# Kernel tuning notes

Measured on AMD Instinct MI355X. Metric: run time of the kernel, lower is better.

## Reference

```python
import jax, jax.numpy as jnp
import numpy as np

BATCH, SEQ, HIDDEN = 8, 2048, 2048
N_FREQS = SEQ // 2 + 1  # 1025


def setup_inputs() -> dict:
    key = jax.random.key(0)
    k_x, k_w, k_b = jax.random.split(key, 3)
    x = jax.random.normal(k_x, (BATCH, SEQ, HIDDEN), dtype=jnp.float32)
    # Params per __init__: gate init ones/zeros; Linear(hidden, hidden)
    gate_real = jnp.ones((N_FREQS, HIDDEN), dtype=jnp.float32)
    gate_imag = jnp.zeros((N_FREQS, HIDDEN), dtype=jnp.float32)
    bound = 1.0 / np.sqrt(HIDDEN)
    W = jax.random.uniform(k_w, (HIDDEN, HIDDEN), minval=-bound, maxval=bound, dtype=jnp.float32)
    b = jax.random.uniform(k_b, (HIDDEN,), minval=-bound, maxval=bound, dtype=jnp.float32)
    return {"x": x, "gate_real": gate_real, "gate_imag": gate_imag, "W": W, "b": b}


def reference(x, gate_real, gate_imag, W, b):
    # x: (batch, seq, hidden)
    seq_len = x.shape[1]
    x_fft = jnp.fft.rfft(x, axis=1)  # (batch, n_freqs, hidden) complex64
    n_freqs = x_fft.shape[1]
    gate = gate_real[:n_freqs] + 1j * gate_imag[:n_freqs]  # (n_freqs, hidden)
    x_fft = x_fft * gate
    y = jnp.fft.irfft(x_fft, n=seq_len, axis=1)  # (batch, seq, hidden) float32
    # out_proj: y @ W.T + b  (torch Linear convention, W: (out, in))
    out = jnp.einsum('bsh,oh->bso', y, W) + b
    return out
```

## Files before the change

kernel.cpp:

```cpp
#include <hip/hip_runtime.h>
#include <math.h>

typedef __attribute__((ext_vector_type(8))) short bf16x8;
typedef __attribute__((ext_vector_type(4))) float f32x4;

__device__ __forceinline__ unsigned short f2bf(float f) {
  unsigned int u = __float_as_uint(f);
  unsigned int r = (u + 0x7fffu + ((u >> 16) & 1u)) >> 16;
  return (unsigned short)r;
}
__device__ __forceinline__ unsigned int pack2bf(float a, float b) {
  return (unsigned int)f2bf(a) | ((unsigned int)f2bf(b) << 16);
}
__device__ __forceinline__ float bflo(unsigned int g) { return __uint_as_float(g << 16); }
__device__ __forceinline__ float bfhi(unsigned int g) { return __uint_as_float(g & 0xffff0000u); }

__device__ __forceinline__ void glds16(const void* gp, void* lp) {
  __builtin_amdgcn_global_load_lds(
      (const __attribute__((address_space(1))) void*)gp,
      (__attribute__((address_space(3))) void*)lp, 16, 0, 0);
}

__device__ __constant__ float CW16[16] = {
  1.0f, 0.9807852804032304f, 0.9238795325112867f, 0.8314696123025452f,
  0.7071067811865476f, 0.5555702330196022f, 0.3826834323650898f, 0.19509032201612828f,
  0.0f, -0.19509032201612828f, -0.3826834323650898f, -0.5555702330196022f,
  -0.7071067811865476f, -0.8314696123025452f, -0.9238795325112867f, -0.9807852804032304f};
__device__ __constant__ float SW16[16] = {
  0.0f, 0.19509032201612828f, 0.3826834323650898f, 0.5555702330196022f,
  0.7071067811865476f, 0.8314696123025452f, 0.9238795325112867f, 0.9807852804032304f,
  1.0f, 0.9807852804032304f, 0.9238795325112867f, 0.8314696123025452f,
  0.7071067811865476f, 0.5555702330196022f, 0.3826834323650898f, 0.19509032201612828f};
__device__ __constant__ int BR5[32] = {
  0,16,8,24,4,20,12,28,2,18,10,26,6,22,14,30,
  1,17,9,25,5,21,13,29,3,19,11,27,7,23,15,31};

__device__ __forceinline__ int bitrev6(int l) {
  return ((l&1)<<5)|((l&2)<<3)|((l&4)<<1)|((l&8)>>1)|((l&16)>>3)|((l&32)>>5);
}

__device__ __forceinline__ float hsin(float rev) { return __builtin_amdgcn_sinf(rev); }
__device__ __forceinline__ float hcos(float rev) { return __builtin_amdgcn_cosf(rev); }

__device__ __forceinline__ void fwd_core(float (&ur)[32], float (&ui)[32], const int lane) {
  #pragma unroll
  for (int s = 0; s < 6; ++s) {
    const int h = 32 >> s;
    const int j = lane & (h - 1);
    const float rev = (float)j * (0.5f / (float)h);
    const bool hi = (lane & h) != 0;
    const float c  = hi ? hcos(rev) : 1.0f;
    const float sv = hi ? hsin(rev) : 0.0f;
    const float sgn = hi ? -1.0f : 1.0f;
    #pragma unroll
    for (int r = 0; r < 32; ++r) {
      float pr = __shfl_xor(ur[r], h, 64);
      float pi = __shfl_xor(ui[r], h, 64);
      float tr = fmaf(sgn, ur[r], pr);
      float ti = fmaf(sgn, ui[r], pi);
      ur[r] = fmaf(ti, sv, tr * c);
      ui[r] = fmaf(-tr, sv, ti * c);
    }
  }
  const int kap = bitrev6(lane);
  #pragma unroll
  for (int j = 1; j < 32; ++j) {
    const float rev = (float)(j * kap) * (1.0f / 2048.0f);
    const float sn = hsin(rev), cs = hcos(rev);
    float t = ur[j] * cs + ui[j] * sn;
    ui[j] = ui[j] * cs - ur[j] * sn;
    ur[j] = t;
  }
  #pragma unroll
  for (int s = 0; s < 5; ++s) {
    const int h = 16 >> s;
    #pragma unroll
    for (int i = 0; i < 32; ++i) if (!(i & h)) {
      const int tw = (i & (h - 1)) * (16 / h);
      float dr = ur[i] - ur[i + h], di = ui[i] - ui[i + h];
      ur[i] += ur[i + h]; ui[i] += ui[i + h];
      ur[i + h] = dr * CW16[tw] + di * SW16[tw];
      ui[i + h] = di * CW16[tw] - dr * SW16[tw];
    }
  }
}

__device__ __forceinline__ void inv_core(float (&ur)[32], float (&ui)[32], const int lane) {
  const int kap = bitrev6(lane);
  #pragma unroll
  for (int s = 0; s < 5; ++s) {
    const int h = 1 << s;
    #pragma unroll
    for (int i = 0; i < 32; ++i) if (!(i & h)) {
      const int tw = (i & (h - 1)) * (16 / h);
      float tr2 = ur[i + h] * CW16[tw] - ui[i + h] * SW16[tw];
      float ti2 = ui[i + h] * CW16[tw] + ur[i + h] * SW16[tw];
      ur[i + h] = ur[i] - tr2; ui[i + h] = ui[i] - ti2;
      ur[i] += tr2; ui[i] += ti2;
    }
  }
  #pragma unroll
  for (int j = 1; j < 32; ++j) {
    const float rev = (float)(j * kap) * (1.0f / 2048.0f);
    const float sn = hsin(rev), cs = hcos(rev);
    float t = ur[j] * cs - ui[j] * sn;
    ui[j] = ui[j] * cs + ur[j] * sn;
    ur[j] = t;
  }
  #pragma unroll
  for (int s = 0; s < 6; ++s) {
    const int h = 1 << s;
    const int j = lane & (h - 1);
    const float rev = (float)j * (0.5f / (float)h);
    const bool hi = (lane & h) != 0;
    const float c  = hi ? hcos(rev) : 1.0f;
    const float sv = hi ? hsin(rev) : 0.0f;
    const float sgn = hi ? -1.0f : 1.0f;
    #pragma unroll
    for (int r = 0; r < 32; ++r) {
      float vr = fmaf(-ui[r], sv, ur[r] * c);
      float vi = fmaf(ur[r], sv, ui[r] * c);
      float pvr = __shfl_xor(vr, h, 64);
      float pvi = __shfl_xor(vi, h, 64);
      ur[r] = fmaf(sgn, vr, pvr);
      ui[r] = fmaf(sgn, vi, pvi);
    }
  }
}

__global__ __launch_bounds__(256) void gate_pack_k(const float* __restrict__ gr,
                                                   const float* __restrict__ gi,
                                                   unsigned int* __restrict__ gt) {
  __shared__ float tr[32][33];
  __shared__ float ti[32][33];
  const int t = threadIdx.x;
  const int k0 = blockIdx.x * 32, hb = blockIdx.y * 32;
  const int hx = t & 31, fr = t >> 5;
  #pragma unroll
  for (int p = 0; p < 4; ++p) {
    int ff = p * 8 + fr;
    int k = k0 + ff;
    int f = (k <= 1024) ? k : (2048 - k);
    float sg = (k <= 1024) ? 1.f : -1.f;
    tr[ff][hx] = gr[(size_t)f * 2048 + hb + hx] * (1.f / 2048.f);
    ti[ff][hx] = sg * gi[(size_t)f * 2048 + hb + hx] * (1.f / 2048.f);
  }
  __syncthreads();
  const int kk = t & 31, hr = t >> 5;
  #pragma unroll
  for (int p = 0; p < 4; ++p) {
    int hl = p * 8 + hr;
    float re = tr[kk][hl], im = ti[kk][hl];
    gt[(size_t)(hb + hl) * 2048 + k0 + kk] =
        (unsigned int)f2bf(re) | ((unsigned int)f2bf(im) << 16);
  }
}

__global__ __launch_bounds__(256) void gate_ab_k(const float* __restrict__ gr,
                                                 const float* __restrict__ gi,
                                                 uint2* __restrict__ ab) {
  __shared__ unsigned int uA[32][33];
  __shared__ unsigned int uB[32][33];
  const int t = threadIdx.x;
  const int k0 = blockIdx.x * 32, h0 = blockIdx.y * 32;
  const int c = t & 31, r = t >> 5;
  #pragma unroll
  for (int pp = 0; pp < 4; ++pp) {
    const int kk = pp * 8 + r;
    const int k = k0 + kk;
    const int h = h0 + c;
    const float gkr = gr[(size_t)k * 2048 + h];
    const float gki = gi[(size_t)k * 2048 + h];
    const float gcr = gr[(size_t)(1024 - k) * 2048 + h];
    const float gci = gi[(size_t)(1024 - k) * 2048 + h];
    const float inv = 1.0f / 1024.0f;
    float Ar, Ai, Br, Bi;
    if (k == 0) {
      Ar = (gkr + gcr) * 0.5f * inv; Ai = 0.f;
      Br = 0.f; Bi = (gkr - gcr) * 0.5f * inv;
    } else {
      const float rev = (float)k * (1.0f / 2048.0f);
      const float sn = hsin(rev), cs = hcos(rev);
      const float Sr = (gkr + gcr) * 0.5f, Si = (gki - gci) * 0.5f;
      const float Dr = (gkr - gcr) * 0.5f, Di = (gki + gci) * 0.5f;
      Ar = (Sr - sn * Dr) * inv; Ai = (Si - sn * Di) * inv;
      Br = (-cs * Di) * inv;     Bi = (cs * Dr) * inv;
    }
    uA[kk][c] = pack2bf(Ar, Ai);
    uB[kk][c] = pack2bf(Br, Bi);
  }
  __syncthreads();
  #pragma unroll
  for (int pp = 0; pp < 4; ++pp) {
    const int hh = pp * 8 + r;
    ab[(size_t)(h0 + hh) * 1024 + k0 + c] = make_uint2(uA[c][hh], uB[c][hh]);
  }
}

__global__ __launch_bounds__(256) void wconv_k(const float* __restrict__ W,
                                               unsigned short* __restrict__ Wb) {
  int i = blockIdx.x * 256 + threadIdx.x;
  float4 v = ((const float4*)W)[i];
  ushort4 o;
  o.x = f2bf(v.x); o.y = f2bf(v.y); o.z = f2bf(v.z); o.w = f2bf(v.w);
  ((ushort4*)Wb)[i] = o;
}

__global__ __launch_bounds__(256) void xtrans_k(const float* __restrict__ x,
                                                float* __restrict__ xT) {
  __shared__ float t[32][33];
  const int b = blockIdx.z;
  const int s0 = blockIdx.x * 32, h0 = blockIdx.y * 32;
  const float* xb = x + ((size_t)b * 2048) * 2048;
  float* xTb = xT + ((size_t)b * 2048) * 2048;
  const int c = threadIdx.x & 31, r = threadIdx.x >> 5;
  #pragma unroll
  for (int p = 0; p < 4; ++p) {
    int rr = p * 8 + r;
    t[rr][c] = xb[(size_t)(s0 + rr) * 2048 + h0 + c];
  }
  __syncthreads();
  #pragma unroll
  for (int p = 0; p < 4; ++p) {
    int rr = p * 8 + r;
    xTb[(size_t)(h0 + rr) * 2048 + s0 + c] = t[c][rr];
  }
}

__global__ __launch_bounds__(256) void ytrans_k(const unsigned short* __restrict__ yT,
                                                unsigned short* __restrict__ y) {
  __shared__ unsigned short t[64][66];
  const int b = blockIdx.z;
  const int h0 = blockIdx.x * 64, s0 = blockIdx.y * 64;
  const unsigned short* src = yT + ((size_t)b * 2048 + h0) * 2048 + s0;
  unsigned short* dst = y + ((size_t)b * 2048 + s0) * 2048 + h0;
  const int c = threadIdx.x & 15, r = threadIdx.x >> 4;
  #pragma unroll
  for (int p = 0; p < 4; ++p) {
    int rr = p * 16 + r;
    ushort4 v = *(const ushort4*)(src + (size_t)rr * 2048 + c * 4);
    *(ushort4*)&t[rr][c * 4] = v;
  }
  __syncthreads();
  #pragma unroll
  for (int p = 0; p < 4; ++p) {
    int rr = p * 16 + r;
    ushort4 o;
    o.x = t[c * 4 + 0][rr]; o.y = t[c * 4 + 1][rr];
    o.z = t[c * 4 + 2][rr]; o.w = t[c * 4 + 3][rr];
    *(ushort4*)(dst + (size_t)rr * 2048 + c * 4) = o;
  }
}

__global__ __attribute__((amdgpu_flat_work_group_size(256, 256)))
__attribute__((amdgpu_waves_per_eu(2, 4)))
void fftr_k(const float* __restrict__ xT,
            const uint2* __restrict__ ab,
            unsigned short* __restrict__ yT) {
  __shared__ float snap[4][32];
  const int tid = threadIdx.x;
  const int w = tid >> 6, lane = tid & 63;
  const size_t col = (size_t)blockIdx.x * 4 + w;
  const int h = (int)(col & 2047);
  const int kap = bitrev6(lane);
  constexpr int BR4[16]   = {0,8,4,12,2,10,6,14,1,9,5,13,3,11,7,15};
  constexpr int P0L16[16] = {0,1,3,2,7,6,5,4,15,14,13,12,11,10,9,8};

  const float4* xc = (const float4*)(xT + col * 2048);
  float4 xv[8];
  #pragma unroll
  for (int q = 0; q < 8; ++q) xv[q] = xc[lane * 8 + q];
  const uint2* abrow = ab + (size_t)h * 1024;
  uint2 abv[16];
  #pragma unroll
  for (int p = 0; p < 16; ++p) abv[p] = abrow[(BR4[p] << 6) + kap];

  float ur[16], ui[16];
  #pragma unroll
  for (int q = 0; q < 8; ++q) {
    ur[2 * q]     = xv[q].x; ui[2 * q]     = xv[q].y;
    ur[2 * q + 1] = xv[q].z; ui[2 * q + 1] = xv[q].w;
  }

  #pragma unroll
  for (int s = 0; s < 6; ++s) {
    const int hh = 32 >> s;
    const int j = lane & (hh - 1);
    const float rev = (float)j * (0.5f / (float)hh);
    const bool hi = (lane & hh) != 0;
    const float c  = hi ? hcos(rev) : 1.0f;
    const float sv = hi ? hsin(rev) : 0.0f;
    const float sgn = hi ? -1.0f : 1.0f;
    #pragma unroll
    for (int r = 0; r < 16; ++r) {
      float pr = __shfl_xor(ur[r], hh, 64);
      float pi = __shfl_xor(ui[r], hh, 64);
      float tr = fmaf(sgn, ur[r], pr);
      float ti = fmaf(sgn, ui[r], pi);
      ur[r] = fmaf(ti, sv, tr * c);
      ui[r] = fmaf(-tr, sv, ti * c);
    }
  }
  #pragma unroll
  for (int j = 1; j < 16; ++j) {
    const float rev = (float)(j * kap) * (1.0f / 1024.0f);
    const float sn = hsin(rev), cs = hcos(rev);
    float t = ur[j] * cs + ui[j] * sn;
    ui[j] = ui[j] * cs - ur[j] * sn;
    ur[j] = t;
  }
  #pragma unroll
  for (int s = 0; s < 4; ++s) {
    const int hh = 8 >> s;
    #pragma unroll
    for (int i = 0; i < 16; ++i) if (!(i & hh)) {
      const int tw = (i & (hh - 1)) * (16 / hh);
      float dr = ur[i] - ur[i + hh], di = ui[i] - ui[i + hh];
      ur[i] += ur[i + hh]; ui[i] += ui[i + hh];
      ur[i + hh] = dr * CW16[tw] + di * SW16[tw];
      ui[i + hh] = di * CW16[tw] - dr * SW16[tw];
    }
  }

  if (lane == 0) {
    #pragma unroll
    for (int p = 0; p < 16; ++p) { snap[w][2 * p] = ur[p]; snap[w][2 * p + 1] = ui[p]; }
  }
  const int lsrc = bitrev6((64 - kap) & 63);
  const bool l0 = (lane == 0);
  #pragma unroll
  for (int c2 = 0; c2 < 4; ++c2) {
    __builtin_amdgcn_sched_barrier(0);
    #pragma unroll
    for (int pp = 0; pp < 2; ++pp) {
      const int p = c2 * 2 + pp;
      const int pb = 15 - p;
      float arp = __shfl(ur[pb], lsrc), aip = __shfl(ui[pb], lsrc);
      float arq = __shfl(ur[p], lsrc),  aiq = __shfl(ui[p], lsrc);
      float s0r = snap[w][2 * P0L16[p]],  s0i = snap[w][2 * P0L16[p] + 1];
      float s1r = snap[w][2 * P0L16[pb]], s1i = snap[w][2 * P0L16[pb] + 1];
      arp = l0 ? s0r : arp;  aip = l0 ? s0i : aip;
      arq = l0 ? s1r : arq;  aiq = l0 ? s1i : aiq;
      {
        float Ar = bflo(abv[p].x), Ai = bfhi(abv[p].x);
        float Br = bflo(abv[p].y), Bi = bfhi(abv[p].y);
        float zr = ur[p], zi = ui[p];
        ur[p] = Ar * zr - Ai * zi + Br * arp + Bi * aip;
        ui[p] = Ar * zi + Ai * zr + Bi * arp - Br * aip;
      }
      {
        float Ar = bflo(abv[pb].x), Ai = bfhi(abv[pb].x);
        float Br = bflo(abv[pb].y), Bi = bfhi(abv[pb].y);
        float zr = ur[pb], zi = ui[pb];
        ur[pb] = Ar * zr - Ai * zi + Br * arq + Bi * aiq;
        ui[pb] = Ar * zi + Ai * zr + Bi * arq - Br * aiq;
      }
    }
  }
  __builtin_amdgcn_sched_barrier(0);

  #pragma unroll
  for (int s = 0; s < 4; ++s) {
    const int hh = 1 << s;
    #pragma unroll
    for (int i = 0; i < 16; ++i) if (!(i & hh)) {
      const int tw = (i & (hh - 1)) * (16 / hh);
      float tr2 = ur[i + hh] * CW16[tw] - ui[i + hh] * SW16[tw];
      float ti2 = ui[i + hh] * CW16[tw] + ur[i + hh] * SW16[tw];
      ur[i + hh] = ur[i] - tr2; ui[i + hh] = ui[i] - ti2;
      ur[i] += tr2; ui[i] += ti2;
    }
  }
  #pragma unroll
  for (int j = 1; j < 16; ++j) {
    const float rev = (float)(j * kap) * (1.0f / 1024.0f);
    const float sn = hsin(rev), cs = hcos(rev);
    float t = ur[j] * cs - ui[j] * sn;
    ui[j] = ui[j] * cs + ur[j] * sn;
    ur[j] = t;
  }
  #pragma unroll
  for (int s = 0; s < 6; ++s) {
    const int hh = 1 << s;
    const int j = lane & (hh - 1);
    const float rev = (float)j * (0.5f / (float)hh);
    const bool hi = (lane & hh) != 0;
    const float c  = hi ? hcos(rev) : 1.0f;
    const float sv = hi ? hsin(rev) : 0.0f;
    const float sgn = hi ? -1.0f : 1.0f;
    #pragma unroll
    for (int r = 0; r < 16; ++r) {
      float vr = fmaf(-ui[r], sv, ur[r] * c);
      float vi = fmaf(ur[r], sv, ui[r] * c);
      float pvr = __shfl_xor(vr, hh, 64);
      float pvi = __shfl_xor(vi, hh, 64);
      ur[r] = fmaf(sgn, vr, pvr);
      ui[r] = fmaf(sgn, vi, pvi);
    }
  }

  uint4* dst = (uint4*)(yT + col * 2048) + lane * 4;
  #pragma unroll
  for (int g = 0; g < 4; ++g) {
    uint4 o;
    o.x = pack2bf(ur[4 * g + 0], ui[4 * g + 0]);
    o.y = pack2bf(ur[4 * g + 1], ui[4 * g + 1]);
    o.z = pack2bf(ur[4 * g + 2], ui[4 * g + 2]);
    o.w = pack2bf(ur[4 * g + 3], ui[4 * g + 3]);
    dst[g] = o;
  }
}

__global__ __attribute__((amdgpu_flat_work_group_size(512, 512)))
__attribute__((amdgpu_waves_per_eu(2, 4)))
void fft_gate_k(const float* __restrict__ x,
                const unsigned int* __restrict__ gt,
                unsigned short* __restrict__ y) {
  __shared__ float lds[8 * 516];
  const int tid = threadIdx.x;
  const int w = tid >> 6;
  const int lane = tid & 63;
  const int bid = blockIdx.x;
  const int swz = (bid & 7) * 256 + (bid >> 3);
  const int h0 = (swz & 255) << 3;
  const int b = swz >> 8;
  const int hh = tid & 7, srow = tid >> 3;

  float ur[32], ui[32];
  const size_t xbase = ((size_t)b * 2048) * 2048 + h0;

  for (int c = 0; c < 4; ++c) {
    #pragma unroll
    for (int q = 0; q < 8; ++q) {
      int soff = q * 64 + srow;
      float v = x[xbase + (size_t)(c * 512 + soff) * 2048 + hh];
      lds[hh * 516 + (soff ^ ((soff >> 5) & 15))] = v;
    }
    __syncthreads();
    if ((lane >> 4) == c) {
      const int li = lane & 15;
      #pragma unroll
      for (int j = 0; j < 32; ++j) {
        ur[j] = lds[w * 516 + ((32 * li + j) ^ li)];
        ui[j] = 0.f;
      }
    }
    __syncthreads();
  }

  fwd_core(ur, ui, lane);
  {
    const int kap = bitrev6(lane);
    const unsigned int* grow = gt + (size_t)(h0 + w) * 2048;
    #pragma unroll
    for (int p = 0; p < 32; ++p) {
      unsigned int g = grow[(BR5[p] << 6) + kap];
      float gre = bflo(g), gim = bfhi(g);
      float t = ur[p] * gre - ui[p] * gim;
      ui[p] = ur[p] * gim + ui[p] * gre;
      ur[p] = t;
    }
  }
  inv_core(ur, ui, lane);

  for (int c = 0; c < 4; ++c) {
    if ((lane >> 4) == c) {
      const int li = lane & 15;
      #pragma unroll
      for (int r = 0; r < 32; ++r)
        lds[w * 516 + ((32 * li + r) ^ li)] = ur[r];
    }
    __syncthreads();
    #pragma unroll
    for (int q = 0; q < 8; ++q) {
      int soff = q * 64 + srow;
      float v = lds[hh * 516 + (soff ^ ((soff >> 5) & 15))];
      y[xbase + (size_t)(c * 512 + soff) * 2048 + hh] = f2bf(v);
    }
    __syncthreads();
  }
}

__global__ __launch_bounds__(256) void gemm_k(const unsigned short* __restrict__ A,
                                              const unsigned short* __restrict__ Bw,
                                              const float* __restrict__ bias,
                                              float* __restrict__ C) {
  __shared__ unsigned short sA[128 * 32];
  __shared__ unsigned short sB[128 * 32];
  const int tid = threadIdx.x;
  const int nwg = gridDim.x;
  const int cpx = nwg >> 3;
  const int bid = blockIdx.x;
  const int swz = (bid & 7) * cpx + (bid >> 3);
  const int bm = swz >> 4, bn = swz & 15;
  const int m0 = bm << 7, n0 = bn << 7;
  const int w = tid >> 6, lane = tid & 63;
  const int arow = tid >> 2, koff = (tid & 3) << 3;
  const unsigned short* gA = A + (size_t)(m0 + arow) * 2048 + koff;
  const unsigned short* gB = Bw + (size_t)(n0 + arow) * 2048 + koff;
  char* sAb = (char*)sA + w * 1024;
  char* sBb = (char*)sB + w * 1024;

  f32x4 acc[4][4];
  #pragma unroll
  for (int i = 0; i < 4; ++i)
    #pragma unroll
    for (int j = 0; j < 4; ++j) acc[i][j] = (f32x4){0.f, 0.f, 0.f, 0.f};

  const int wr = w >> 1, wc = w & 1;
  const int row16 = lane & 15, kb = lane >> 4;

  for (int k0 = 0; k0 < 2048; k0 += 32) {
    glds16(gA + k0, sAb);
    glds16(gA + 64 * 2048 + k0, sAb + 4096);
    glds16(gB + k0, sBb);
    glds16(gB + 64 * 2048 + k0, sBb + 4096);
    __syncthreads();
    bf16x8 af[4], bfr[4];
    #pragma unroll
    for (int i = 0; i < 4; ++i) {
      int r = (wr << 6) + (i << 4) + row16;
      af[i] = *(const bf16x8*)(sA + r * 32 + (kb << 3));
    }
    #pragma unroll
    for (int j2 = 0; j2 < 4; ++j2) {
      int r = (wc << 6) + (j2 << 4) + row16;
      bfr[j2] = *(const bf16x8*)(sB + r * 32 + (kb << 3));
    }
    #pragma unroll
    for (int i = 0; i < 4; ++i)
      #pragma unroll
      for (int j2 = 0; j2 < 4; ++j2)
        acc[i][j2] = __builtin_amdgcn_mfma_f32_16x16x32_bf16(af[i], bfr[j2], acc[i][j2], 0, 0, 0);
    __syncthreads();
  }

  const int rq = lane >> 4;
  #pragma unroll
  for (int j2 = 0; j2 < 4; ++j2) {
    int oc = n0 + (wc << 6) + (j2 << 4) + row16;
    float bj = bias[oc];
    #pragma unroll
    for (int i = 0; i < 4; ++i) {
      int mr = m0 + (wr << 6) + (i << 4) + (rq << 2);
      #pragma unroll
      for (int q = 0; q < 4; ++q)
        C[(size_t)(mr + q) * 2048 + oc] = acc[i][j2][q] + bj;
    }
  }
}

__global__ __launch_bounds__(512) void gemm8_k(const unsigned short* __restrict__ A,
                                               const unsigned short* __restrict__ Bw,
                                               const float* __restrict__ bias,
                                               float* __restrict__ C) {
  extern __shared__ char lds[];
  const int tid = threadIdx.x;
  const int w = tid >> 6, lane = tid & 63;
  const int bid = blockIdx.x;
  const int swz = (bid & 7) * 64 + (bid >> 3);
  const int m0 = (swz >> 3) << 8;
  const int n0 = (swz & 7) << 8;
  const int wr = w >> 2, wc = w & 3;
  const int row16 = lane & 15, kb = lane >> 4;

  const int lr = lane >> 2, ls = lane & 3;
  const int r0 = (w << 5) + lr, r1 = r0 + 16;
  const unsigned short* pA0 = A  + (size_t)(m0 + r0) * 2048 + ((ls ^ ((r0 >> 1) & 3)) << 3);
  const unsigned short* pA1 = A  + (size_t)(m0 + r1) * 2048 + ((ls ^ ((r1 >> 1) & 3)) << 3);
  const unsigned short* pB0 = Bw + (size_t)(n0 + r0) * 2048 + ((ls ^ ((r0 >> 1) & 3)) << 3);
  const unsigned short* pB1 = Bw + (size_t)(n0 + r1) * 2048 + ((ls ^ ((r1 >> 1) & 3)) << 3);
  const int dW = w << 11;

  f32x4 acc[8][4];
  #pragma unroll
  for (int i = 0; i < 8; ++i)
    #pragma unroll
    for (int j = 0; j < 4; ++j) acc[i][j] = (f32x4){0.f, 0.f, 0.f, 0.f};

  auto STAGE_A = [&](int t) {
    char* base = lds + ((t & 3) << 15);
    const int k0 = t << 5;
    glds16(pA0 + k0, base + dW);
    glds16(pA1 + k0, base + dW + 1024);
  };
  auto STAGE_B = [&](int t) {
    char* base = lds + ((t & 3) << 15);
    const int k0 = t << 5;
    glds16(pB0 + k0, base + 16384 + dW);
    glds16(pB1 + k0, base + 16384 + dW + 1024);
  };
  auto LDA4 = [&](const char* base, int i0, bf16x8 (&af)[4]) {
    #pragma unroll
    for (int i = 0; i < 4; ++i) {
      const int r = (wr << 7) + ((i0 + i) << 4) + row16;
      af[i] = *(const bf16x8*)(base + (r << 6) + ((kb ^ ((r >> 1) & 3)) << 4));
    }
  };
  auto LDB4 = [&](const char* base, bf16x8 (&bfr)[4]) {
    #pragma unroll
    for (int j = 0; j < 4; ++j) {
      const int r = (wc << 6) + (j << 4) + row16;
      bfr[j] = *(const bf16x8*)(base + 16384 + (r << 6) + ((kb ^ ((r >> 1) & 3)) << 4));
    }
  };
  auto MM16 = [&](const bf16x8 (&af)[4], const bf16x8 (&bfr)[4], int i0) {
    #pragma unroll
    for (int i = 0; i < 4; ++i)
      #pragma unroll
      for (int j = 0; j < 4; ++j)
        acc[i0 + i][j] = __builtin_amdgcn_mfma_f32_16x16x32_bf16(af[i], bfr[j], acc[i0 + i][j], 0, 0, 0);
  };
  auto COMPUTE = [&](int t) {
    const char* base = lds + ((t & 3) << 15);
    bf16x8 af[4], af2[4], bfr[4];
    LDA4(base, 0, af); LDA4(base, 4, af2); LDB4(base, bfr);
    MM16(af, bfr, 0); MM16(af2, bfr, 4);
  };

  STAGE_A(0); STAGE_B(0); STAGE_A(1); STAGE_B(1); STAGE_A(2); STAGE_B(2);
  asm volatile("s_waitcnt vmcnt(8)" ::: "memory");
  __builtin_amdgcn_s_barrier();
  __builtin_amdgcn_sched_barrier(0);

  for (int t = 0; t < 61; ++t) {
    const char* base = lds + ((t & 3) << 15);
    bf16x8 af[4], bfr[4];
    LDA4(base, 0, af);
    LDB4(base, bfr);
    STAGE_A(t + 3);
    asm volatile("s_waitcnt lgkmcnt(0)" ::: "memory");
    __builtin_amdgcn_sched_barrier(0);
    __builtin_amdgcn_s_setprio(1);
    MM16(af, bfr, 0);
    __builtin_amdgcn_s_setprio(0);
    __builtin_amdgcn_s_barrier();
    bf16x8 af2[4];
    LDA4(base, 4, af2);
    STAGE_B(t + 3);
    asm volatile("s_waitcnt lgkmcnt(0)" ::: "memory");
    __builtin_amdgcn_sched_barrier(0);
    __builtin_amdgcn_s_setprio(1);
    MM16(af2, bfr, 4);
    __builtin_amdgcn_s_setprio(0);
    asm volatile("s_waitcnt vmcnt(8)" ::: "memory");
    __builtin_amdgcn_s_barrier();
    __builtin_amdgcn_sched_barrier(0);
  }
  COMPUTE(61);
  asm volatile("s_waitcnt vmcnt(4)" ::: "memory");
  __builtin_amdgcn_s_barrier();
  __builtin_amdgcn_sched_barrier(0);
  COMPUTE(62);
  asm volatile("s_waitcnt vmcnt(0)" ::: "memory");
  __builtin_amdgcn_s_barrier();
  __builtin_amdgcn_sched_barrier(0);
  COMPUTE(63);

  const int rq = lane >> 4;
  #pragma unroll
  for (int j = 0; j < 4; ++j) {
    const int oc = n0 + (wc << 6) + (j << 4) + row16;
    const float bj = bias[oc];
    #pragma unroll
    for (int i = 0; i < 8; ++i) {
      const int mr = m0 + (wr << 7) + (i << 4) + (rq << 2);
      #pragma unroll
      for (int q = 0; q < 4; ++q)
        C[(size_t)(mr + q) * 2048 + oc] = acc[i][j][q] + bj;
    }
  }
}

extern "C" void kernel_launch(void* const* d_in, const int* in_sizes, int n_in,
                              void* d_out, int out_size, void* d_ws, size_t ws_size,
                              hipStream_t stream) {
  const float* x  = (const float*)d_in[0];
  const float* gr = (const float*)d_in[1];
  const float* gi = (const float*)d_in[2];
  const float* W  = (const float*)d_in[3];
  const float* bs = (const float*)d_in[4];
  float* out = (float*)d_out;

  char* ws = (char*)d_ws;
  unsigned short* yb = (unsigned short*)ws;
  unsigned short* Wb = (unsigned short*)(ws + (64ull << 20));
  unsigned int*   gt = (unsigned int*)(ws + (72ull << 20));
  uint2*          ab = (uint2*)(ws + (72ull << 20));
  float*          xT = (float*)(ws + (88ull << 20));
  unsigned short* yT = (unsigned short*)(ws + (216ull << 20));
  const bool fast = ws_size >= (280ull << 20);

  hipLaunchKernelGGL(wconv_k, dim3(4096), dim3(256), 0, stream, W, Wb);
  if (fast) {
    hipLaunchKernelGGL(gate_ab_k, dim3(32, 64), dim3(256), 0, stream, gr, gi, ab);
    hipLaunchKernelGGL(xtrans_k, dim3(64, 64, 8), dim3(256), 0, stream, x, xT);
    hipLaunchKernelGGL(fftr_k, dim3(4096), dim3(256), 0, stream, xT, ab, yT);
    hipLaunchKernelGGL(ytrans_k, dim3(32, 32, 8), dim3(256), 0, stream, yT, yb);
  } else {
    hipLaunchKernelGGL(gate_pack_k, dim3(64, 64), dim3(256), 0, stream, gr, gi, gt);
    hipLaunchKernelGGL(fft_gate_k, dim3(2048), dim3(512), 0, stream, x, gt, yb);
  }

  const bool big = hipFuncSetAttribute((const void*)gemm8_k,
                                       hipFuncAttributeMaxDynamicSharedMemorySize,
                                       131072) == hipSuccess;
  if (big) {
    hipLaunchKernelGGL(gemm8_k, dim3(512), dim3(512), 131072, stream, yb, Wb, bs, out);
  } else {
    hipLaunchKernelGGL(gemm_k, dim3(2048), dim3(256), 0, stream, yb, Wb, bs, out);
  }
}
```

Measured before the change: 350.1 us.

## Store transposed input as bf16 and stage gate coefficients through LDS

The transpose kernel now writes its intermediate in bf16 rather than fp32, using 64x64 tiles with float4 loads and 16-byte packed stores. This halves the transposed buffer traffic for both its write and the FFT kernel's read. The FFT kernel now copies the per-column gate coefficients into shared memory with async global-to-LDS loads instead of holding 16 uint2 values in registers, which reduces register pressure. The cost is rounding the FFT input to bf16, which lowers accuracy, plus extra LDS use per block.

After: 337.2 us, median of 2. 1.04x faster.

```diff
diff --git a/kernel.cpp b/kernel.cpp
--- a/kernel.cpp
+++ b/kernel.cpp
@@ -207,23 +207,33 @@
 }
 
 __global__ __launch_bounds__(256) void xtrans_k(const float* __restrict__ x,
-                                                float* __restrict__ xT) {
-  __shared__ float t[32][33];
+                                                unsigned short* __restrict__ xT) {
+  __shared__ float t[64][65];
   const int b = blockIdx.z;
-  const int s0 = blockIdx.x * 32, h0 = blockIdx.y * 32;
+  const int s0 = blockIdx.x * 64, h0 = blockIdx.y * 64;
   const float* xb = x + ((size_t)b * 2048) * 2048;
-  float* xTb = xT + ((size_t)b * 2048) * 2048;
-  const int c = threadIdx.x & 31, r = threadIdx.x >> 5;
+  unsigned short* xTb = xT + ((size_t)b * 2048) * 2048;
+  const int c4 = (threadIdx.x & 15) * 4;
+  const int r0 = threadIdx.x >> 4;
   #pragma unroll
   for (int p = 0; p < 4; ++p) {
-    int rr = p * 8 + r;
-    t[rr][c] = xb[(size_t)(s0 + rr) * 2048 + h0 + c];
+    const int rr = p * 16 + r0;
+    float4 v = *(const float4*)(xb + (size_t)(s0 + rr) * 2048 + h0 + c4);
+    t[rr][c4 + 0] = v.x; t[rr][c4 + 1] = v.y;
+    t[rr][c4 + 2] = v.z; t[rr][c4 + 3] = v.w;
   }
   __syncthreads();
-  #pragma unroll
-  for (int p = 0; p < 4; ++p) {
-    int rr = p * 8 + r;
-    xTb[(size_t)(h0 + rr) * 2048 + s0 + c] = t[c][rr];
+  const int j = threadIdx.x & 7;
+  const int hr0 = threadIdx.x >> 3;
+  #pragma unroll
+  for (int p = 0; p < 2; ++p) {
+    const int hh = p * 32 + hr0;
+    uint4 o;
+    o.x = pack2bf(t[j * 8 + 0][hh], t[j * 8 + 1][hh]);
+    o.y = pack2bf(t[j * 8 + 2][hh], t[j * 8 + 3][hh]);
+    o.z = pack2bf(t[j * 8 + 4][hh], t[j * 8 + 5][hh]);
+    o.w = pack2bf(t[j * 8 + 6][hh], t[j * 8 + 7][hh]);
+    *(uint4*)(xTb + (size_t)(h0 + hh) * 2048 + s0 + j * 8) = o;
   }
 }
 
@@ -254,10 +264,11 @@
 
 __global__ __attribute__((amdgpu_flat_work_group_size(256, 256)))
 __attribute__((amdgpu_waves_per_eu(2, 4)))
-void fftr_k(const float* __restrict__ xT,
+void fftr_k(const unsigned short* __restrict__ xT,
             const uint2* __restrict__ ab,
             unsigned short* __restrict__ yT) {
   __shared__ float snap[4][32];
+  __shared__ uint2 labs[4][1024];
   const int tid = threadIdx.x;
   const int w = tid >> 6, lane = tid & 63;
   const size_t col = (size_t)blockIdx.x * 4 + w;
@@ -266,20 +277,25 @@
   constexpr int BR4[16]   = {0,8,4,12,2,10,6,14,1,9,5,13,3,11,7,15};
   constexpr int P0L16[16] = {0,1,3,2,7,6,5,4,15,14,13,12,11,10,9,8};
 
-  const float4* xc = (const float4*)(xT + col * 2048);
-  float4 xv[8];
-  #pragma unroll
-  for (int q = 0; q < 8; ++q) xv[q] = xc[lane * 8 + q];
-  const uint2* abrow = ab + (size_t)h * 1024;
-  uint2 abv[16];
-  #pragma unroll
-  for (int p = 0; p < 16; ++p) abv[p] = abrow[(BR4[p] << 6) + kap];
+  {
+    const char* gsrc = (const char*)(ab + (size_t)h * 1024);
+    char* ldst = (char*)&labs[w][0];
+    #pragma unroll
+    for (int p8 = 0; p8 < 8; ++p8)
+      glds16(gsrc + p8 * 1024 + lane * 16, ldst + p8 * 1024);
+  }
 
   float ur[16], ui[16];
-  #pragma unroll
-  for (int q = 0; q < 8; ++q) {
-    ur[2 * q]     = xv[q].x; ui[2 * q]     = xv[q].y;
-    ur[2 * q + 1] = xv[q].z; ui[2 * q + 1] = xv[q].w;
+  {
+    const unsigned short* xc = xT + col * 2048;
+    #pragma unroll
+    for (int q = 0; q < 4; ++q) {
+      uint4 v = *(const uint4*)(xc + lane * 32 + q * 8);
+      ur[4 * q + 0] = bflo(v.x); ui[4 * q + 0] = bfhi(v.x);
+      ur[4 * q + 1] = bflo(v.y); ui[4 * q + 1] = bfhi(v.y);
+      ur[4 * q + 2] = bflo(v.z); ui[4 * q + 2] = bfhi(v.z);
+      ur[4 * q + 3] = bflo(v.w); ui[4 * q + 3] = bfhi(v.w);
+    }
   }
 
   #pragma unroll
@@ -326,6 +342,7 @@
     #pragma unroll
     for (int p = 0; p < 16; ++p) { snap[w][2 * p] = ur[p]; snap[w][2 * p + 1] = ui[p]; }
   }
+  asm volatile("s_waitcnt vmcnt(0)" ::: "memory");
   const int lsrc = bitrev6((64 - kap) & 63);
   const bool l0 = (lane == 0);
   #pragma unroll
@@ -341,16 +358,16 @@
       float s1r = snap[w][2 * P0L16[pb]], s1i = snap[w][2 * P0L16[pb] + 1];
       arp = l0 ? s0r : arp;  aip = l0 ? s0i : aip;
       arq = l0 ? s1r : arq;  aiq = l0 ? s1i : aiq;
+      uint2 gp = labs[w][(BR4[p]  << 6) + kap];
+      uint2 gq = labs[w][(BR4[pb] << 6) + kap];
       {
-        float Ar = bflo(abv[p].x), Ai = bfhi(abv[p].x);
-        float Br = bflo(abv[p].y), Bi = bfhi(abv[p].y);
+        float Ar = bflo(gp.x), Ai = bfhi(gp.x), Br = bflo(gp.y), Bi = bfhi(gp.y);
         float zr = ur[p], zi = ui[p];
         ur[p] = Ar * zr - Ai * zi + Br * arp + Bi * aip;
         ui[p] = Ar * zi + Ai * zr + Bi * arp - Br * aip;
       }
       {
-        float Ar = bflo(abv[pb].x), Ai = bfhi(abv[pb].x);
-        float Br = bflo(abv[pb].y), Bi = bfhi(abv[pb].y);
+        float Ar = bflo(gq.x), Ai = bfhi(gq.x), Br = bflo(gq.y), Bi = bfhi(gq.y);
         float zr = ur[pb], zi = ui[pb];
         ur[pb] = Ar * zr - Ai * zi + Br * arq + Bi * aiq;
         ui[pb] = Ar * zi + Ai * zr + Bi * arq - Br * aiq;
@@ -687,14 +704,14 @@
   unsigned short* Wb = (unsigned short*)(ws + (64ull << 20));
   unsigned int*   gt = (unsigned int*)(ws + (72ull << 20));
   uint2*          ab = (uint2*)(ws + (72ull << 20));
-  float*          xT = (float*)(ws + (88ull << 20));
+  unsigned short* xT = (unsigned short*)(ws + (88ull << 20));
   unsigned short* yT = (unsigned short*)(ws + (216ull << 20));
   const bool fast = ws_size >= (280ull << 20);
 
   hipLaunchKernelGGL(wconv_k, dim3(4096), dim3(256), 0, stream, W, Wb);
   if (fast) {
     hipLaunchKernelGGL(gate_ab_k, dim3(32, 64), dim3(256), 0, stream, gr, gi, ab);
-    hipLaunchKernelGGL(xtrans_k, dim3(64, 64, 8), dim3(256), 0, stream, x, xT);
+    hipLaunchKernelGGL(xtrans_k, dim3(32, 32, 8), dim3(256), 0, stream, x, xT);
     hipLaunchKernelGGL(fftr_k, dim3(4096), dim3(256), 0, stream, xT, ab, yT);
     hipLaunchKernelGGL(ytrans_k, dim3(32, 32, 8), dim3(256), 0, stream, yT, yb);
   } else {
```
